# Kernel tuning notes

Measured on AMD Instinct MI355X. Metric: run time of the kernel, lower is better.

## Reference

```python
import jax, jax.numpy as jnp
import numpy as np

TEMPERATURE = 0.07
C_MARGIN = 0.5
T_MARGIN = 1.0
GAMMA = 2.0
ALPHA = 0.25
SMOOTHING = 0.1
W_CONTRASTIVE = 0.1
W_TRIPLET = 0.1
W_FOCAL = 0.4
W_LABEL_SMOOTH = 0.4


def setup_inputs() -> dict:
    key = jax.random.key(0)
    k1, k2, k3 = jax.random.split(key, 3)
    B, C, D = 2048, 1000, 512
    pred = jax.random.normal(k1, (B, C), dtype=jnp.float32)
    target = jax.random.randint(k2, (B,), 0, C, dtype=jnp.int64)
    features = jax.random.normal(k3, (B, D), dtype=jnp.float32)
    return {"pred": pred, "target": target, "features": features}


def _safe_cdist(f):
    # Euclidean pairwise distance with zero-grad at zero distance (matches torch.cdist on diagonal).
    r = jnp.sum(f * f, axis=1)
    d2 = jnp.maximum(r[:, None] - 2.0 * (f @ f.T) + r[None, :], 0.0)
    pos = d2 > 0
    return jnp.sqrt(jnp.where(pos, d2, 1.0)) * pos


def _contrastive(features, labels):
    f = features / jnp.linalg.norm(features, axis=1, keepdims=True)
    sim = f @ f.T  # [B, B]
    lm = (labels[:, None] == labels[None, :]).astype(sim.dtype)
    pos = sim * lm
    pos_loss = -jnp.log(jnp.exp(pos / TEMPERATURE) + 1e-8)
    neg = sim * (1.0 - lm)
    neg_loss = jnp.maximum(C_MARGIN - neg, 0.0)
    return pos_loss.mean() + neg_loss.mean()


def _triplet(features, labels):
    B = features.shape[0]
    d = _safe_cdist(features)  # [B, B]
    lm = (labels[:, None] == labels[None, :]).astype(d.dtype)
    pm, nm = lm, 1.0 - lm

    def body(acc, args):
        di, pmi, nmi = args  # [B], [B], [B]
        # sum over (p, n): relu(d_ip - d_in + margin), masked
        contrib = jnp.sum(
            jnp.maximum(di[:, None] - di[None, :] + T_MARGIN, 0.0)
            * pmi[:, None] * nmi[None, :]
        )
        return acc + contrib, None

    loss, _ = jax.lax.scan(body, jnp.float32(0.0), (d, pm, nm))
    return loss / (B + 1e-8)


def _focal(pred, target):
    logp = jax.nn.log_softmax(pred, axis=1)
    ce = -jnp.take_along_axis(logp, target[:, None], axis=1)[:, 0]
    pt = jnp.exp(-ce)
    return (ALPHA * (1.0 - pt) ** GAMMA * ce).mean()


def _label_smoothing(pred, target):
    C = pred.shape[1]
    off = SMOOTHING / (C - 1)
    logp = jax.nn.log_softmax(pred, axis=1)
    # smooth target: off everywhere, (1 - smoothing) at target index
    tgt_logp = jnp.take_along_axis(logp, target[:, None], axis=1)[:, 0]
    loss = -(off * logp.sum(axis=1) + ((1.0 - SMOOTHING) - off) * tgt_logp)
    return loss.mean()


def reference(pred, target, features):
    lc = _contrastive(features, target)
    lt = _triplet(features, target)
    lf = _focal(pred, target)
    ls = _label_smoothing(pred, target)
    total = (W_CONTRASTIVE * lc + W_TRIPLET * lt
             + W_FOCAL * lf + W_LABEL_SMOOTH * ls)
    return jnp.stack([lc, lt, lf, ls, total])
```

## Files before the change

kernel.cpp:

```cpp
#include <hip/hip_runtime.h>
#include <hip/hip_bf16.h>
#include <math.h>

typedef __attribute__((ext_vector_type(8))) short bf16x8;
typedef __attribute__((ext_vector_type(4))) float f32x4;

static constexpr float TEMP_INV  = 1.0f / 0.07f;
static constexpr float C_MARGIN  = 0.5f;
static constexpr float T_MARGIN  = 1.0f;
static constexpr float ALPHA     = 0.25f;
static constexpr float SMOOTHING = 0.1f;
static constexpr float LSE_SHIFT = 8.0f;

__device__ __forceinline__ unsigned short f2bf(float x) {
    __hip_bfloat16 h = __float2bfloat16(x);
    return *reinterpret_cast<unsigned short*>(&h);
}
__device__ __forceinline__ float bf2f(unsigned short u) {
    union { unsigned int u32; float f; } U;
    U.u32 = ((unsigned int)u) << 16;
    return U.f;
}
__device__ __forceinline__ bf16x8 pack8(float4 a, float4 b) {
    bf16x8 r;
    r[0] = (short)f2bf(a.x); r[1] = (short)f2bf(a.y);
    r[2] = (short)f2bf(a.z); r[3] = (short)f2bf(a.w);
    r[4] = (short)f2bf(b.x); r[5] = (short)f2bf(b.y);
    r[6] = (short)f2bf(b.z); r[7] = (short)f2bf(b.w);
    return r;
}

__global__ __launch_bounds__(256) void gram_ce_kernel(
    const float* __restrict__ F, unsigned short* __restrict__ Gb,
    const float* __restrict__ pred, const int* __restrict__ target,
    float* __restrict__ partialCE, float* __restrict__ diag,
    float* __restrict__ inv_norm, int B, int D, int C, float off_const,
    int tilesX) {
    __shared__ unsigned short As[128 * 32];
    __shared__ unsigned short Bs[128 * 32];
    __shared__ float red[12];

    const int nTiles = tilesX * tilesX;
    const int tid = threadIdx.x;
    const int lane = tid & 63, wid = tid >> 6;

    if (blockIdx.x < nTiles) {
        const int rowBase = (blockIdx.x / tilesX) * 128;
        const int colBase = (blockIdx.x % tilesX) * 128;
        const int wr = (wid >> 1) * 64;
        const int wc = (wid & 1) * 64;
        const int half = lane >> 4;
        const int rr   = lane & 15;

        const float* FA = F + (size_t)rowBase * D;
        const float* FB = F + (size_t)colBase * D;

        int r2_[2]; int ldo_[2]; size_t go_[2];
#pragma unroll
        for (int c = 0; c < 2; ++c) {
            const int chunk = c * 256 + tid;
            const int r2 = chunk >> 2, q = chunk & 3;
            r2_[c]  = r2;
            ldo_[c] = r2 * 32 + ((q ^ (r2 & 3)) * 8);
            go_[c]  = (size_t)r2 * D + q * 8;
        }

        f32x4 acc[4][4];
#pragma unroll
        for (int m = 0; m < 4; ++m)
#pragma unroll
            for (int n = 0; n < 4; ++n) acc[m][n] = (f32x4){0.f, 0.f, 0.f, 0.f};

        for (int k0 = 0; k0 < D; k0 += 32) {
#pragma unroll
            for (int c = 0; c < 2; ++c) {
                float4 a0 = *(const float4*)(FA + go_[c] + k0);
                float4 a1 = *(const float4*)(FA + go_[c] + k0 + 4);
                float4 b0 = *(const float4*)(FB + go_[c] + k0);
                float4 b1 = *(const float4*)(FB + go_[c] + k0 + 4);
                *(bf16x8*)(&As[ldo_[c]]) = pack8(a0, a1);
                *(bf16x8*)(&Bs[ldo_[c]]) = pack8(b0, b1);
            }
            __syncthreads();
            bf16x8 af[4], bfv[4];
#pragma unroll
            for (int f = 0; f < 4; ++f) {
                const int ar = wr + f * 16 + rr;
                af[f]  = *(const bf16x8*)(&As[ar * 32 + ((half ^ (ar & 3)) * 8)]);
                const int br = wc + f * 16 + rr;
                bfv[f] = *(const bf16x8*)(&Bs[br * 32 + ((half ^ (br & 3)) * 8)]);
            }
#pragma unroll
            for (int m = 0; m < 4; ++m)
#pragma unroll
                for (int n = 0; n < 4; ++n)
                    acc[m][n] = __builtin_amdgcn_mfma_f32_16x16x32_bf16(
                        af[m], bfv[n], acc[m][n], 0, 0, 0);
            __syncthreads();
        }
#pragma unroll
        for (int m = 0; m < 4; ++m) {
            const int i0 = rowBase + wr + m * 16 + half * 4;
#pragma unroll
            for (int n = 0; n < 4; ++n) {
                const int j = colBase + wc + n * 16 + rr;
#pragma unroll
                for (int r = 0; r < 4; ++r)
                    Gb[(size_t)(i0 + r) * B + j] = f2bf(acc[m][n][r]);
            }
        }
    } else {
        const int i = blockIdx.x - nTiles;
        const float2* Fr2 = (const float2*)(F + (size_t)i * D);
        float ns = 0.0f;
        for (int idx = tid; idx < (D >> 1); idx += 256) {
            float2 f = Fr2[idx];
            ns += f.x * f.x + f.y * f.y;
        }
        const float* prow = pred + (size_t)i * C;
        const float tlogit = prow[target[i]];
        const int Cv = C >> 2;
        float s = 0.0f, sp = 0.0f;
        for (int idx = tid; idx < Cv; idx += 256) {
            float4 v = ((const float4*)prow)[idx];
            s += expf(v.x - LSE_SHIFT) + expf(v.y - LSE_SHIFT)
               + expf(v.z - LSE_SHIFT) + expf(v.w - LSE_SHIFT);
            sp += v.x + v.y + v.z + v.w;
        }
        for (int j = Cv * 4 + tid; j < C; j += 256) {
            float v = prow[j];
            s += expf(v - LSE_SHIFT);
            sp += v;
        }
#pragma unroll
        for (int off = 32; off > 0; off >>= 1) {
            s  += __shfl_down(s, off, 64);
            sp += __shfl_down(sp, off, 64);
            ns += __shfl_down(ns, off, 64);
        }
        if (lane == 0) { red[wid] = s; red[4 + wid] = sp; red[8 + wid] = ns; }
        __syncthreads();
        if (tid == 0) {
            float sT  = red[0] + red[1] + red[2] + red[3];
            float spT = red[4] + red[5] + red[6] + red[7];
            float nsT = red[8] + red[9] + red[10] + red[11];
            float lse = LSE_SHIFT + logf(sT);
            float tl  = tlogit - lse;
            float ce  = -tl;
            float pt  = expf(tl);
            float omp = 1.0f - pt;
            float focal = ALPHA * omp * omp * ce;
            float sumlogp = spT - (float)C * lse;
            float lsv = -(off_const * sumlogp + ((1.0f - SMOOTHING) - off_const) * tl);
            partialCE[(size_t)i * 2]     = focal;
            partialCE[(size_t)i * 2 + 1] = lsv;
            diag[i] = nsT;
            inv_norm[i] = 1.0f / sqrtf(nsT);
        }
    }
}

__global__ __launch_bounds__(256) void row_loss_kernel(
    const unsigned short* __restrict__ Gb, const float* __restrict__ diag,
    const float* __restrict__ inv_norm, const int* __restrict__ labels,
    float* __restrict__ partial, int B) {
    __shared__ float p_d[256];
    __shared__ float red[12];
    __shared__ int p_cnt;
    const int tid = threadIdx.x;
    const int i = blockIdx.x;
    const int j0 = tid * 8;

    union { uint4 u; unsigned short s[8]; } GV;
    GV.u = *(const uint4*)(Gb + (size_t)i * B + j0);
    int lab[8];
    *(int4*)&lab[0] = *(const int4*)(labels + j0);
    *(int4*)&lab[4] = *(const int4*)(labels + j0 + 4);
    float dg[8], ivn[8];
    *(float4*)&dg[0]  = *(const float4*)(diag + j0);
    *(float4*)&dg[4]  = *(const float4*)(diag + j0 + 4);
    *(float4*)&ivn[0] = *(const float4*)(inv_norm + j0);
    *(float4*)&ivn[4] = *(const float4*)(inv_norm + j0 + 4);
    const int   li     = labels[i];
    const float ri     = diag[i];
    const float inv_ni = inv_norm[i];

    if (tid == 0) p_cnt = 0;
    __syncthreads();

    float pos = 0.0f, neg = 0.0f;
    float d8[8];
    int mmask = 0;
#pragma unroll
    for (int e = 0; e < 8; ++e) {
        const int j = j0 + e;
        const float g = bf2f(GV.s[e]);
        float sim = g * inv_ni * ivn[e];
        const float d2 = ri - 2.0f * g + dg[e];
        float d = (d2 > 0.0f) ? sqrtf(d2) : 0.0f;
        if (j == i) { sim = 1.0f; d = 0.0f; }
        d8[e] = d;
        if (lab[e] == li) {
            pos += -logf(expf(sim * TEMP_INV) + 1e-8f);
            neg += C_MARGIN;
            mmask |= (1 << e);
            int slot = atomicAdd(&p_cnt, 1);
            if (slot < 256) p_d[slot] = d;
        } else {
            neg += fmaxf(C_MARGIN - sim, 0.0f);
        }
    }
    __syncthreads();
    const int cnt = (p_cnt < 256) ? p_cnt : 256;
    float trip = 0.0f;
    for (int p = 0; p < cnt; ++p) {
        const float dp = p_d[p] + T_MARGIN;
#pragma unroll
        for (int e = 0; e < 8; ++e)
            if (!(mmask & (1 << e))) trip += fmaxf(dp - d8[e], 0.0f);
    }

    float r0 = pos, r1 = neg, r2 = trip;
#pragma unroll
    for (int off = 32; off > 0; off >>= 1) {
        r0 += __shfl_down(r0, off, 64);
        r1 += __shfl_down(r1, off, 64);
        r2 += __shfl_down(r2, off, 64);
    }
    const int lane = tid & 63, wid = tid >> 6;
    if (lane == 0) { red[wid] = r0; red[4 + wid] = r1; red[8 + wid] = r2; }
    __syncthreads();
    if (tid == 0) {
        float4 o;
        o.x = red[0] + red[1] + red[2] + red[3];
        o.y = red[4] + red[5] + red[6] + red[7];
        o.z = red[8] + red[9] + red[10] + red[11];
        o.w = 0.0f;
        *(float4*)(partial + (size_t)i * 4) = o;
    }
}

__global__ __launch_bounds__(1024) void reduce_kernel(
    const float* __restrict__ partialT, const float* __restrict__ partialCE,
    float* __restrict__ out, int B) {
    __shared__ float red[16][5];
    const int tid = threadIdx.x;
    float s[5] = {0.f, 0.f, 0.f, 0.f, 0.f};
    for (int r = tid; r < B; r += 1024) {
        float4 v = *(const float4*)(partialT + (size_t)r * 4);
        s[0] += v.x; s[1] += v.y; s[2] += v.z;
    }
    for (int t = tid; t < (B * 2) / 4; t += 1024) {
        float4 v = *(const float4*)(partialCE + (size_t)t * 4);
        s[3] += v.x + v.z; s[4] += v.y + v.w;
    }
#pragma unroll
    for (int off = 32; off > 0; off >>= 1) {
#pragma unroll
        for (int k = 0; k < 5; ++k) s[k] += __shfl_down(s[k], off, 64);
    }
    const int lane = tid & 63, wid = tid >> 6;
    if (lane == 0) {
#pragma unroll
        for (int k = 0; k < 5; ++k) red[wid][k] = s[k];
    }
    __syncthreads();
    if (tid == 0) {
        float t[5];
#pragma unroll
        for (int k = 0; k < 5; ++k) {
            t[k] = red[0][k];
#pragma unroll
            for (int q = 1; q < 16; ++q) t[k] += red[q][k];
        }
        double invB2 = 1.0 / ((double)B * (double)B);
        float lc = (float)(((double)t[0] + (double)t[1]) * invB2);
        float lt = (float)((double)t[2] / ((double)B + 1e-8));
        float lf = t[3] / (float)B;
        float ls = t[4] / (float)B;
        out[0] = lc;
        out[1] = lt;
        out[2] = lf;
        out[3] = ls;
        out[4] = 0.1f * lc + 0.1f * lt + 0.4f * lf + 0.4f * ls;
    }
}

extern "C" void kernel_launch(void* const* d_in, const int* in_sizes, int n_in,
                              void* d_out, int out_size, void* d_ws, size_t ws_size,
                              hipStream_t stream) {
    const float* pred     = (const float*)d_in[0];
    const int*   target   = (const int*)d_in[1];
    const float* features = (const float*)d_in[2];
    const int B = in_sizes[1];
    const int C = in_sizes[0] / B;
    const int D = in_sizes[2] / B;
    float* out = (float*)d_out;
    const int tilesX = B / 128;
    const int nTiles = tilesX * tilesX;

    float* partial   = (float*)d_ws;
    float* partialCE = partial + (size_t)B * 4;
    float* diag      = partialCE + (size_t)B * 2;
    float* inv_norm  = diag + B;
    unsigned short* Gb = (unsigned short*)(inv_norm + B);

    float off_const = SMOOTHING / (float)(C - 1);
    gram_ce_kernel<<<nTiles + B, 256, 0, stream>>>(
        features, Gb, pred, target, partialCE, diag, inv_norm,
        B, D, C, off_const, tilesX);

    row_loss_kernel<<<B, 256, 0, stream>>>(Gb, diag, inv_norm, target,
                                           partial, B);

    reduce_kernel<<<1, 1024, 0, stream>>>(partial, partialCE, out, B);
}
```

Before: 36.91 us.

## Double-buffer shared memory tiles in Gram GEMM with register prefetch

The Gram-matrix GEMM loop now uses two LDS buffers. Each iteration prefetches the next k-slice of global fp32 features into registers before running the MFMAs on the current buffer, then converts and stores the prefetched data into the other buffer. This removes one __syncthreads per iteration and overlaps global load latency with matrix math. The cost is double the LDS footprint and more live registers, which may reduce occupancy.

```diff
diff --git a/kernel.cpp b/kernel.cpp
--- a/kernel.cpp
+++ b/kernel.cpp
@@ -36,8 +36,8 @@
     float* __restrict__ partialCE, float* __restrict__ diag,
     float* __restrict__ inv_norm, int B, int D, int C, float off_const,
     int tilesX) {
-    __shared__ unsigned short As[128 * 32];
-    __shared__ unsigned short Bs[128 * 32];
+    __shared__ unsigned short As[2][128 * 32];
+    __shared__ unsigned short Bs[2][128 * 32];
     __shared__ float red[12];
 
     const int nTiles = tilesX * tilesX;
@@ -55,12 +55,11 @@
         const float* FA = F + (size_t)rowBase * D;
         const float* FB = F + (size_t)colBase * D;
 
-        int r2_[2]; int ldo_[2]; size_t go_[2];
+        int ldo_[2]; size_t go_[2];
 #pragma unroll
         for (int c = 0; c < 2; ++c) {
             const int chunk = c * 256 + tid;
             const int r2 = chunk >> 2, q = chunk & 3;
-            r2_[c]  = r2;
             ldo_[c] = r2 * 32 + ((q ^ (r2 & 3)) * 8);
             go_[c]  = (size_t)r2 * D + q * 8;
         }
@@ -71,24 +70,42 @@
 #pragma unroll
             for (int n = 0; n < 4; ++n) acc[m][n] = (f32x4){0.f, 0.f, 0.f, 0.f};
 
-        for (int k0 = 0; k0 < D; k0 += 32) {
-#pragma unroll
-            for (int c = 0; c < 2; ++c) {
-                float4 a0 = *(const float4*)(FA + go_[c] + k0);
-                float4 a1 = *(const float4*)(FA + go_[c] + k0 + 4);
-                float4 b0 = *(const float4*)(FB + go_[c] + k0);
-                float4 b1 = *(const float4*)(FB + go_[c] + k0 + 4);
-                *(bf16x8*)(&As[ldo_[c]]) = pack8(a0, a1);
-                *(bf16x8*)(&Bs[ldo_[c]]) = pack8(b0, b1);
+        float4 pa0[2], pa1[2], pb0[2], pb1[2];
+
+#pragma unroll
+        for (int c = 0; c < 2; ++c) {
+            pa0[c] = *(const float4*)(FA + go_[c]);
+            pa1[c] = *(const float4*)(FA + go_[c] + 4);
+            pb0[c] = *(const float4*)(FB + go_[c]);
+            pb1[c] = *(const float4*)(FB + go_[c] + 4);
+        }
+#pragma unroll
+        for (int c = 0; c < 2; ++c) {
+            *(bf16x8*)(&As[0][ldo_[c]]) = pack8(pa0[c], pa1[c]);
+            *(bf16x8*)(&Bs[0][ldo_[c]]) = pack8(pb0[c], pb1[c]);
+        }
+        __syncthreads();
+
+        const int NT = D / 32;
+        for (int t = 0; t < NT; ++t) {
+            const int cur = t & 1;
+            if (t + 1 < NT) {
+                const int k1 = (t + 1) * 32;
+#pragma unroll
+                for (int c = 0; c < 2; ++c) {
+                    pa0[c] = *(const float4*)(FA + go_[c] + k1);
+                    pa1[c] = *(const float4*)(FA + go_[c] + k1 + 4);
+                    pb0[c] = *(const float4*)(FB + go_[c] + k1);
+                    pb1[c] = *(const float4*)(FB + go_[c] + k1 + 4);
+                }
             }
-            __syncthreads();
             bf16x8 af[4], bfv[4];
 #pragma unroll
             for (int f = 0; f < 4; ++f) {
                 const int ar = wr + f * 16 + rr;
-                af[f]  = *(const bf16x8*)(&As[ar * 32 + ((half ^ (ar & 3)) * 8)]);
+                af[f]  = *(const bf16x8*)(&As[cur][ar * 32 + ((half ^ (ar & 3)) * 8)]);
                 const int br = wc + f * 16 + rr;
-                bfv[f] = *(const bf16x8*)(&Bs[br * 32 + ((half ^ (br & 3)) * 8)]);
+                bfv[f] = *(const bf16x8*)(&Bs[cur][br * 32 + ((half ^ (br & 3)) * 8)]);
             }
 #pragma unroll
             for (int m = 0; m < 4; ++m)
@@ -96,6 +113,13 @@
                 for (int n = 0; n < 4; ++n)
                     acc[m][n] = __builtin_amdgcn_mfma_f32_16x16x32_bf16(
                         af[m], bfv[n], acc[m][n], 0, 0, 0);
+            if (t + 1 < NT) {
+#pragma unroll
+                for (int c = 0; c < 2; ++c) {
+                    *(bf16x8*)(&As[cur ^ 1][ldo_[c]]) = pack8(pa0[c], pa1[c]);
+                    *(bf16x8*)(&Bs[cur ^ 1][ldo_[c]]) = pack8(pb0[c], pb1[c]);
+                }
+            }
             __syncthreads();
         }
 #pragma unroll
```

Measured after the change: 31.77 us. -13.9%, faster.
